# Performance work log

Measured on AMD Instinct MI355X. Metric: run time of the kernel, lower is better.

## Reference

```python
import jax, jax.numpy as jnp
import numpy as np

N, D, NBINS, NUM_IDS = 8192, 256, 64, 512
MAX_DIST = 2.0  # initial +/- histogram range from __init__ (max_dist default)
EPS_DIST = 1e-12
EPS_HIST = 1e-6


def setup_inputs() -> dict:
    key = jax.random.key(0)
    kx, kt = jax.random.split(key)
    x = jax.random.normal(kx, (N, D), dtype=jnp.float32)
    targets = jax.random.randint(kt, (N,), 0, NUM_IDS, dtype=jnp.int64)
    histogram = jnp.ones((NBINS,), dtype=jnp.float32)  # buffer initial state
    return {"x": x, "targets": targets, "histogram": histogram}


def reference(x, targets, histogram):
    n = x.shape[0]
    nbins = histogram.shape[0]
    # pairwise euclidean distances: [n, n]
    sq = jnp.sum(x * x, axis=1)
    dist = jnp.sqrt(jnp.clip(sq[:, None] + sq[None, :] - 2.0 * (x @ x.T), EPS_DIST, None))
    mask = targets[:, None] == targets[None, :]
    neg_inf = jnp.array(-jnp.inf, dtype=dist.dtype)
    pos_inf = jnp.array(jnp.inf, dtype=dist.dtype)
    pos_dist = jnp.max(jnp.where(mask, dist, neg_inf), axis=1)  # hardest positive per row
    neg_dist = jnp.min(jnp.where(mask, pos_inf, dist), axis=1)  # hardest negative per row
    hist_val = pos_dist - neg_dist
    # _compute_histogram: widen range by batch extremes (torch uses .item() on detached values)
    hv = jax.lax.stop_gradient(hist_val)
    max_val = jnp.maximum(jnp.max(hv), MAX_DIST)
    min_val = jnp.minimum(jnp.min(hv), -MAX_DIST)
    bin_width = (max_val - min_val) / (nbins - 1)
    lo = jnp.floor((hv - min_val) / bin_width).astype(jnp.int32)
    hi = jnp.clip(lo + 1, 0, nbins - 1)
    alpha = 1.0 - (hv - min_val - lo.astype(hv.dtype) * bin_width) / bin_width
    hist = jnp.zeros((nbins,), dtype=hv.dtype).at[lo].add(alpha).at[hi].add(1.0 - alpha)
    hist = hist / (jnp.sum(hist) + EPS_HIST)
    # first call: _stats_initialized is False -> momentum = 1.0, new buffer = hist
    new_histogram = hist
    pdf = new_histogram / jnp.sum(new_histogram)
    cdf = jnp.cumsum(pdf)
    bin_idx = jnp.floor((hv - min_val) / bin_width).astype(jnp.int32)
    weight = cdf[bin_idx]  # detached weighting (built entirely from stop_gradient values)
    loss = -jnp.mean(neg_dist * weight) + jnp.mean(pos_dist * weight)
    return loss
```

## Files before the change

kernel.cpp:

```cpp
#include <hip/hip_runtime.h>
#include <math.h>

#define Nn 8192
#define Dd 256
#define NBINS 64
#define NSPLIT 8

typedef __attribute__((ext_vector_type(8))) short short8;
typedef __attribute__((ext_vector_type(4))) float f32x4;

#define GLOAD16(g, l)                                                        \
  __builtin_amdgcn_global_load_lds(                                          \
      (const __attribute__((address_space(1))) void*)(g),                    \
      (__attribute__((address_space(3))) void*)(l), 16, 0, 0)

static __device__ __forceinline__ unsigned short f2bf(float f) {
  unsigned int u = __float_as_uint(f);
  u = (u + 0x7fffu + ((u >> 16) & 1u)) >> 16;
  return (unsigned short)u;
}
static __device__ __forceinline__ unsigned int enc_ord(float f) {
  unsigned int u = __float_as_uint(f);
  return (u & 0x80000000u) ? ~u : (u | 0x80000000u);
}
static __device__ __forceinline__ float dec_ord(unsigned int u) {
  unsigned int b2 = (u & 0x80000000u) ? (u ^ 0x80000000u) : ~u;
  return __uint_as_float(b2);
}

__global__ __launch_bounds__(256) void prep_kernel(const float* __restrict__ x,
                                                   const int* __restrict__ lab,
                                                   unsigned short* __restrict__ xb,
                                                   float2* __restrict__ sqlab,
                                                   unsigned int* __restrict__ pos2,
                                                   unsigned int* __restrict__ neg2,
                                                   unsigned int* __restrict__ gmm,
                                                   float* __restrict__ ghist,
                                                   float* __restrict__ ghsum) {
  const int w = threadIdx.x >> 6;
  const int lane = threadIdx.x & 63;
  const int row = blockIdx.x * 4 + w;
  const float4 v = *(const float4*)(x + (size_t)row * Dd + lane * 4);
  ushort4 b;
  b.x = f2bf(v.x); b.y = f2bf(v.y); b.z = f2bf(v.z); b.w = f2bf(v.w);
  *(ushort4*)(xb + (size_t)row * Dd + lane * 4) = b;
  float s = v.x * v.x + v.y * v.y + v.z * v.z + v.w * v.w;
#pragma unroll
  for (int off = 32; off >= 1; off >>= 1) s += __shfl_xor(s, off);
  if (lane == 0) {
    sqlab[row] = make_float2(s, __int_as_float(lab[row]));
    pos2[row] = 0x007fffffu;
    neg2[row] = 0xff800000u;
  }
  if (blockIdx.x == 0 && threadIdx.x < NBINS) {
    ghist[threadIdx.x] = 0.0f;
    ghsum[threadIdx.x] = 0.0f;
    if (threadIdx.x == 0) { gmm[0] = 0x007fffffu; gmm[1] = 0xff800000u; }
  }
}

static __device__ __forceinline__ void stage_a(const unsigned short* __restrict__ xb,
                                               int r0, int hh, unsigned short* buf, int t) {
#pragma unroll
  for (int i = 0; i < 8; ++i) {
    const int c = i * 256 + t;
    const int col = c >> 4;
    const int kq = (c & 15) ^ (col & 15);
    GLOAD16(xb + (size_t)(r0 + col) * Dd + hh * 128 + kq * 8, buf + (size_t)c * 8);
  }
}
static __device__ __forceinline__ void stage_b(const unsigned short* __restrict__ xb,
                                               int c0, int hh, unsigned short* buf, int t) {
#pragma unroll
  for (int i = 0; i < 4; ++i) {
    const int c = i * 256 + t;
    const int col = c >> 4;
    const int kq = (c & 15) ^ (col & 15);
    GLOAD16(xb + (size_t)(c0 + col) * Dd + hh * 128 + kq * 8, buf + (size_t)c * 8);
  }
}

__global__ __launch_bounds__(256, 2) void pairwise_kernel(const unsigned short* __restrict__ xb,
                                                          const float2* __restrict__ sqlab,
                                                          unsigned int* __restrict__ pos2,
                                                          unsigned int* __restrict__ neg2) {
  __shared__ __align__(16) unsigned short Us[4096 * 8];
  __shared__ __align__(16) float2 sl_s[1024];
  __shared__ int lab_s[128];

  const int t = threadIdx.x;
  const int lane = t & 63;
  const int w = t >> 6;
  const int wr = w >> 1;
  const int wc = w & 1;
  const int c_l = lane & 15;
  const int kq_l = lane >> 4;
  const int rows0 = blockIdx.x * 128;
  const int cbase = blockIdx.y * (Nn / NSPLIT);

  stage_a(xb, rows0, 0, Us, t);
  stage_a(xb, rows0, 1, Us + 2048 * 8, t);
#pragma unroll
  for (int i = 0; i < 4; ++i) sl_s[i * 256 + t] = sqlab[cbase + i * 256 + t];
  if (t < 128) lab_s[t] = __float_as_int(sqlab[rows0 + t].y);
  __syncthreads();

  const short8* Uv = (const short8*)Us;
  short8 af[32];
#pragma unroll
  for (int k2 = 0; k2 < 8; ++k2)
#pragma unroll
    for (int m = 0; m < 4; ++m) {
      const int kqf = k2 * 4 + kq_l;
      const int rl = wr * 64 + m * 16 + c_l;
      af[k2 * 4 + m] = Uv[(kqf >> 4) * 2048 + rl * 16 + ((kqf & 15) ^ (rl & 15))];
    }
  int labp[8];
#pragma unroll
  for (int m = 0; m < 4; ++m)
#pragma unroll
    for (int pp = 0; pp < 2; ++pp) {
      const int r0 = wr * 64 + m * 16 + kq_l * 4 + 2 * pp;
      labp[m * 2 + pp] = (lab_s[r0] & 0xffff) | (lab_s[r0 + 1] << 16);
    }
  __syncthreads();

  unsigned short* const B0 = Us;
  unsigned short* const B1 = Us + 1024 * 8;
  unsigned short* const B2 = Us + 2048 * 8;

  stage_b(xb, cbase, 0, B0, t);
  stage_b(xb, cbase, 1, B1, t);

  const int cc0 = wc * 32 + c_l;
  const int cc1 = wc * 32 + 16 + c_l;
  float pmax[16], nmin[16];
#pragma unroll
  for (int i = 0; i < 16; ++i) { pmax[i] = -INFINITY; nmin[i] = INFINITY; }

  int rA = 0;
#pragma unroll 1
  for (int ct = 0; ct < 16; ++ct) {
    const int rB = (rA == 2) ? 0 : rA + 1;
    const int rC = (rB == 2) ? 0 : rB + 1;
    unsigned short* const bufA = (rA == 0) ? B0 : ((rA == 1) ? B1 : B2);
    unsigned short* const bufB = (rB == 0) ? B0 : ((rB == 1) ? B1 : B2);
    unsigned short* const bufC = (rC == 0) ? B0 : ((rC == 1) ? B1 : B2);
    const int cnext = cbase + ((ct + 1) & 15) * 64;

    f32x4 acc[4][2];
#pragma unroll
    for (int m = 0; m < 4; ++m)
#pragma unroll
      for (int n = 0; n < 2; ++n) acc[m][n] = (f32x4){0.f, 0.f, 0.f, 0.f};

    asm volatile("s_waitcnt vmcnt(4)" ::: "memory");
    __builtin_amdgcn_s_barrier();
    stage_b(xb, cnext, 0, bufC, t);
    {
      const short8* Bv = (const short8*)bufA;
#pragma unroll
      for (int ks = 0; ks < 4; ++ks) {
        const short8 bf0 = Bv[cc0 * 16 + ((ks * 4 + kq_l) ^ (cc0 & 15))];
        const short8 bf1 = Bv[cc1 * 16 + ((ks * 4 + kq_l) ^ (cc1 & 15))];
#pragma unroll
        for (int m = 0; m < 4; ++m) {
          acc[m][0] = __builtin_amdgcn_mfma_f32_16x16x32_bf16(af[ks * 4 + m], bf0, acc[m][0], 0, 0, 0);
          acc[m][1] = __builtin_amdgcn_mfma_f32_16x16x32_bf16(af[ks * 4 + m], bf1, acc[m][1], 0, 0, 0);
        }
      }
    }

    asm volatile("s_waitcnt vmcnt(4)" ::: "memory");
    __builtin_amdgcn_s_barrier();
    stage_b(xb, cnext, 1, bufA, t);
    {
      const short8* Bv = (const short8*)bufB;
#pragma unroll
      for (int ks = 0; ks < 4; ++ks) {
        const short8 bf0 = Bv[cc0 * 16 + ((ks * 4 + kq_l) ^ (cc0 & 15))];
        const short8 bf1 = Bv[cc1 * 16 + ((ks * 4 + kq_l) ^ (cc1 & 15))];
#pragma unroll
        for (int m = 0; m < 4; ++m) {
          acc[m][0] = __builtin_amdgcn_mfma_f32_16x16x32_bf16(af[(4 + ks) * 4 + m], bf0, acc[m][0], 0, 0, 0);
          acc[m][1] = __builtin_amdgcn_mfma_f32_16x16x32_bf16(af[(4 + ks) * 4 + m], bf1, acc[m][1], 0, 0, 0);
        }
      }
    }

    {
      const float2 sl0 = sl_s[ct * 64 + cc0];
      const float2 sl1 = sl_s[ct * 64 + cc1];
#pragma unroll
      for (int n = 0; n < 2; ++n) {
        const float sc = (n == 0) ? sl0.x : sl1.x;
        const int lc = __float_as_int((n == 0) ? sl0.y : sl1.y);
#pragma unroll
        for (int idx = 0; idx < 16; ++idx) {
          const int m = idx >> 2, q = idx & 3;
          const float g = fmaf(-2.0f, acc[m][n][q], sc);
          const int lr = (labp[idx >> 1] >> ((idx & 1) * 16)) & 0xffff;
          const bool same = (lr == lc);
          pmax[idx] = same ? fmaxf(pmax[idx], g) : pmax[idx];
          nmin[idx] = same ? nmin[idx] : fminf(nmin[idx], g);
        }
      }
    }
    rA = rC;
  }

#pragma unroll
  for (int i = 0; i < 16; ++i) {
    float p = pmax[i], nn2 = nmin[i];
#pragma unroll
    for (int off = 1; off < 16; off <<= 1) {
      p = fmaxf(p, __shfl_xor(p, off));
      nn2 = fminf(nn2, __shfl_xor(nn2, off));
    }
    if (c_l == 0) {
      const int rowg = rows0 + wr * 64 + (i >> 2) * 16 + kq_l * 4 + (i & 3);
      atomicMax(&pos2[rowg], enc_ord(p));
      atomicMin(&neg2[rowg], enc_ord(nn2));
    }
  }
}

__global__ __launch_bounds__(512) void finalize_a_kernel(const float2* __restrict__ sqlab,
                                                         const unsigned int* __restrict__ pos2,
                                                         const unsigned int* __restrict__ neg2,
                                                         float* __restrict__ hv_g,
                                                         unsigned int* __restrict__ gmm) {
  const int i = blockIdx.x * 512 + threadIdx.x;
  const int lane = threadIdx.x & 63;
  const float s = sqlab[i].x;
  const float p2 = fmaxf(s + dec_ord(pos2[i]), 1e-12f);
  const float n2 = fmaxf(s + dec_ord(neg2[i]), 1e-12f);
  const float hv = sqrtf(p2) - sqrtf(n2);
  hv_g[i] = hv;
  float lmax = hv, lmin = hv;
#pragma unroll
  for (int off = 32; off >= 1; off >>= 1) {
    lmax = fmaxf(lmax, __shfl_xor(lmax, off));
    lmin = fminf(lmin, __shfl_xor(lmin, off));
  }
  if (lane == 0) {
    atomicMax(&gmm[0], enc_ord(lmax));
    atomicMin(&gmm[1], enc_ord(lmin));
  }
}

__global__ __launch_bounds__(512) void finalize_b_kernel(const float* __restrict__ hv_g,
                                                         const unsigned int* __restrict__ gmm,
                                                         float* __restrict__ ghist,
                                                         float* __restrict__ ghsum) {
  __shared__ float hist_s[NBINS];
  __shared__ float hsum_s[NBINS];
  const int t = threadIdx.x;
  if (t < NBINS) { hist_s[t] = 0.0f; hsum_s[t] = 0.0f; }
  const float maxv = fmaxf(dec_ord(gmm[0]), 2.0f);
  const float minv = fminf(dec_ord(gmm[1]), -2.0f);
  const float bw = (maxv - minv) / (float)(NBINS - 1);
  __syncthreads();

  const int i = blockIdx.x * 512 + t;
  const float hv = hv_g[i];
  int lo = (int)floorf((hv - minv) / bw);
  lo = min(max(lo, 0), NBINS - 1);
  const int hi = min(lo + 1, NBINS - 1);
  const float alpha = 1.0f - (hv - minv - (float)lo * bw) / bw;
  atomicAdd(&hist_s[lo], alpha);
  atomicAdd(&hist_s[hi], 1.0f - alpha);
  atomicAdd(&hsum_s[lo], hv);
  __syncthreads();

  if (t < NBINS) {
    atomicAdd(&ghist[t], hist_s[t]);
    atomicAdd(&ghsum[t], hsum_s[t]);
  }
}

__global__ __launch_bounds__(64) void finalize_c_kernel(const float* __restrict__ ghist,
                                                        const float* __restrict__ ghsum,
                                                        float* __restrict__ out) {
  const int t = threadIdx.x;
  const float h = ghist[t];
  float total = h;
#pragma unroll
  for (int off = 32; off >= 1; off >>= 1) total += __shfl_xor(total, off);
  const float hn = h / (total + 1e-6f);
  float s2 = hn;
#pragma unroll
  for (int off = 32; off >= 1; off >>= 1) s2 += __shfl_xor(s2, off);
  const float pdf = hn / s2;
  float c = pdf;
#pragma unroll
  for (int off = 1; off < 64; off <<= 1) {
    const float u = __shfl_up(c, off);
    if (t >= off) c += u;
  }
  float acc = c * ghsum[t];
#pragma unroll
  for (int off = 32; off >= 1; off >>= 1) acc += __shfl_xor(acc, off);
  if (t == 0) out[0] = acc / (float)Nn;
}

extern "C" void kernel_launch(void* const* d_in, const int* in_sizes, int n_in,
                              void* d_out, int out_size, void* d_ws, size_t ws_size,
                              hipStream_t stream) {
  const float* x = (const float*)d_in[0];
  const int* targets = (const int*)d_in[1];
  float* out = (float*)d_out;

  char* p = (char*)d_ws;
  unsigned short* xb = (unsigned short*)p;  p += (size_t)Nn * Dd * 2;
  float2* sqlab = (float2*)p;               p += (size_t)Nn * 8;
  unsigned int* pos2 = (unsigned int*)p;    p += (size_t)Nn * 4;
  unsigned int* neg2 = (unsigned int*)p;    p += (size_t)Nn * 4;
  float* hv_g = (float*)p;                  p += (size_t)Nn * 4;
  unsigned int* gmm = (unsigned int*)p;     p += 64;
  float* ghist = (float*)p;                 p += NBINS * 4;
  float* ghsum = (float*)p;

  prep_kernel<<<Nn / 4, 256, 0, stream>>>(x, targets, xb, sqlab, pos2, neg2, gmm, ghist, ghsum);
  pairwise_kernel<<<dim3(Nn / 128, NSPLIT), 256, 0, stream>>>(xb, sqlab, pos2, neg2);
  finalize_a_kernel<<<Nn / 512, 512, 0, stream>>>(sqlab, pos2, neg2, hv_g, gmm);
  finalize_b_kernel<<<Nn / 512, 512, 0, stream>>>(hv_g, gmm, ghist, ghsum);
  finalize_c_kernel<<<1, 64, 0, stream>>>(ghist, ghsum, out);
}
```

Measured before the change: 64.51 us.

## Exploit distance-matrix symmetry to compute only upper-triangular tiles

Uses the symmetry of the pairwise distance matrix so each block handles only column tiles at or above its row tile, and also reduces column-wise max/min into shared-memory arrays that are merged into the global positive and negative results with atomics. Block indices are remapped to pair short and long rows to balance load, and excess blocks exit early. This roughly halves the MFMA work in exchange for extra per-column reductions, shuffles, LDS atomics and global atomics, plus some load imbalance across blocks.

```diff
diff --git a/kernel.cpp b/kernel.cpp
--- a/kernel.cpp
+++ b/kernel.cpp
@@ -4,7 +4,6 @@
 #define Nn 8192
 #define Dd 256
 #define NBINS 64
-#define NSPLIT 8
 
 typedef __attribute__((ext_vector_type(8))) short short8;
 typedef __attribute__((ext_vector_type(4))) float f32x4;
@@ -85,7 +84,7 @@
                                                           unsigned int* __restrict__ pos2,
                                                           unsigned int* __restrict__ neg2) {
   __shared__ __align__(16) unsigned short Us[4096 * 8];
-  __shared__ __align__(16) float2 sl_s[1024];
+  __shared__ float rowsl[128];
   __shared__ int lab_s[128];
 
   const int t = threadIdx.x;
@@ -95,14 +94,22 @@
   const int wc = w & 1;
   const int c_l = lane & 15;
   const int kq_l = lane >> 4;
-  const int rows0 = blockIdx.x * 128;
-  const int cbase = blockIdx.y * (Nn / NSPLIT);
+
+  const int s = blockIdx.x & 7;
+  const int q = blockIdx.x >> 3;
+  const int bi = (q & 1) ? (63 - (q >> 1)) : (q >> 1);
+  const int rows0 = bi * 128;
+  const int c0 = 2 * bi + ((s - 2 * bi) & 7);
+  if (c0 >= 128) return;
+  const int nct = (128 - c0 + 7) >> 3;
 
   stage_a(xb, rows0, 0, Us, t);
   stage_a(xb, rows0, 1, Us + 2048 * 8, t);
-#pragma unroll
-  for (int i = 0; i < 4; ++i) sl_s[i * 256 + t] = sqlab[cbase + i * 256 + t];
-  if (t < 128) lab_s[t] = __float_as_int(sqlab[rows0 + t].y);
+  if (t < 128) {
+    const float2 v = sqlab[rows0 + t];
+    rowsl[t] = v.x;
+    lab_s[t] = __float_as_int(v.y);
+  }
   __syncthreads();
 
   const short8* Uv = (const short8*)Us;
@@ -128,9 +135,23 @@
   unsigned short* const B0 = Us;
   unsigned short* const B1 = Us + 1024 * 8;
   unsigned short* const B2 = Us + 2048 * 8;
-
-  stage_b(xb, cbase, 0, B0, t);
-  stage_b(xb, cbase, 1, B1, t);
+  unsigned int* const colP = (unsigned int*)(Us + 24576);
+  unsigned int* const colN = (unsigned int*)(Us + 26624);
+  float2* const slv = (float2*)(Us + 28672);
+
+#pragma unroll
+  for (int i = 0; i < 4; ++i) {
+    colP[i * 256 + t] = 0x007fffffu;
+    colN[i * 256 + t] = 0xff800000u;
+  }
+  for (int i = t; i < nct * 64; i += 256) {
+    const int cc = c0 + 8 * (i >> 6);
+    slv[i] = sqlab[cc * 64 + (i & 63)];
+  }
+  __syncthreads();
+
+  stage_b(xb, c0 * 64, 0, B0, t);
+  stage_b(xb, c0 * 64, 1, B1, t);
 
   const int cc0 = wc * 32 + c_l;
   const int cc1 = wc * 32 + 16 + c_l;
@@ -140,13 +161,14 @@
 
   int rA = 0;
 #pragma unroll 1
-  for (int ct = 0; ct < 16; ++ct) {
+  for (int o = 0; o < nct; ++o) {
+    const int c = c0 + 8 * o;
     const int rB = (rA == 2) ? 0 : rA + 1;
     const int rC = (rB == 2) ? 0 : rB + 1;
     unsigned short* const bufA = (rA == 0) ? B0 : ((rA == 1) ? B1 : B2);
     unsigned short* const bufB = (rB == 0) ? B0 : ((rB == 1) ? B1 : B2);
     unsigned short* const bufC = (rC == 0) ? B0 : ((rC == 1) ? B1 : B2);
-    const int cnext = cbase + ((ct + 1) & 15) * 64;
+    const int cnext = ((o + 1 < nct) ? (c + 8) : c0) * 64;
 
     f32x4 acc[4][2];
 #pragma unroll
@@ -189,24 +211,43 @@
     }
 
     {
-      const float2 sl0 = sl_s[ct * 64 + cc0];
-      const float2 sl1 = sl_s[ct * 64 + cc1];
+      const float2 sl0 = slv[o * 64 + cc0];
+      const float2 sl1 = slv[o * 64 + cc1];
 #pragma unroll
       for (int n = 0; n < 2; ++n) {
         const float sc = (n == 0) ? sl0.x : sl1.x;
         const int lc = __float_as_int((n == 0) ? sl0.y : sl1.y);
+        float wp = -INFINITY, wn = INFINITY;
 #pragma unroll
         for (int idx = 0; idx < 16; ++idx) {
-          const int m = idx >> 2, q = idx & 3;
-          const float g = fmaf(-2.0f, acc[m][n][q], sc);
+          const int m = idx >> 2, qq = idx & 3;
+          const float a2 = acc[m][n][qq];
           const int lr = (labp[idx >> 1] >> ((idx & 1) * 16)) & 0xffff;
           const bool same = (lr == lc);
+          const float g = fmaf(-2.0f, a2, sc);
           pmax[idx] = same ? fmaxf(pmax[idx], g) : pmax[idx];
           nmin[idx] = same ? nmin[idx] : fminf(nmin[idx], g);
+          const float wv = fmaf(-2.0f, a2, rowsl[wr * 64 + m * 16 + kq_l * 4 + qq]);
+          wp = same ? fmaxf(wp, wv) : wp;
+          wn = same ? wn : fminf(wn, wv);
+        }
+        wp = fmaxf(wp, __shfl_xor(wp, 16)); wp = fmaxf(wp, __shfl_xor(wp, 32));
+        wn = fminf(wn, __shfl_xor(wn, 16)); wn = fminf(wn, __shfl_xor(wn, 32));
+        if (lane < 16) {
+          const int ci = o * 64 + ((n == 0) ? cc0 : cc1);
+          atomicMax(&colP[ci], enc_ord(wp));
+          atomicMin(&colN[ci], enc_ord(wn));
         }
       }
     }
     rA = rC;
+  }
+
+  __syncthreads();
+  for (int i = t; i < nct * 64; i += 256) {
+    const int colg = (c0 + 8 * (i >> 6)) * 64 + (i & 63);
+    atomicMax(&pos2[colg], colP[i]);
+    atomicMin(&neg2[colg], colN[i]);
   }
 
 #pragma unroll
@@ -322,7 +363,7 @@
   float* ghsum = (float*)p;
 
   prep_kernel<<<Nn / 4, 256, 0, stream>>>(x, targets, xb, sqlab, pos2, neg2, gmm, ghist, ghsum);
-  pairwise_kernel<<<dim3(Nn / 128, NSPLIT), 256, 0, stream>>>(xb, sqlab, pos2, neg2);
+  pairwise_kernel<<<512, 256, 0, stream>>>(xb, sqlab, pos2, neg2);
   finalize_a_kernel<<<Nn / 512, 512, 0, stream>>>(sqlab, pos2, neg2, hv_g, gmm);
   finalize_b_kernel<<<Nn / 512, 512, 0, stream>>>(hv_g, gmm, ghist, ghsum);
   finalize_c_kernel<<<1, 64, 0, stream>>>(ghist, ghsum, out);
```

Result: slower. 78.71 us (+22.0%).
